# Kernel tuning notes

Measured on AMD Instinct MI355X. Metric: run time of the kernel, lower is better.

## Reference

```python
import jax, jax.numpy as jnp
import numpy as np


def setup_inputs() -> dict:
    key = jax.random.key(0)
    kx, kw = jax.random.split(key)
    x = jax.random.normal(kx, (32, 128, 64, 64), dtype=jnp.float32)
    weights = jax.random.normal(kw, (256, 128, 3, 3), dtype=jnp.float32) * 0.05
    return {"x": x, "weights": weights}


def reference(x, weights):
    # Valid-padding, stride-1, no-bias 2D cross-correlation, identical math
    # to the nested-loop HandmadeConv2d (sum over in_ch, kH, kW per output pixel).
    return jax.lax.conv_general_dilated(
        x, weights,
        window_strides=(1, 1),
        padding="VALID",
        dimension_numbers=("NCHW", "OIHW", "NCHW"),
    )
```

## Files before the change

kernel.cpp:

```cpp
#include <hip/hip_runtime.h>
#include <hip/hip_bf16.h>

typedef unsigned short ushort;
typedef unsigned int uint;
typedef __bf16 bf16x8 __attribute__((ext_vector_type(8)));
typedef float f32x4 __attribute__((ext_vector_type(4)));
typedef uint uint4v __attribute__((ext_vector_type(4)));
typedef uint uint2v __attribute__((ext_vector_type(2)));

#define CI 128
#define HIN 64
#define WIN 64
#define CO 256
#define HO 62
#define WO 62
#define NB 32
#define KTOT 1152
#define PIXIMG 3844
#define NPIX 123008
#define XIMG 524288
#define BK 64
#define NKT 18

__device__ __forceinline__ ushort f2bf(float f) {
  uint u = __builtin_bit_cast(uint, f);
  u += 0x7fffu + ((u >> 16) & 1u);
  return (ushort)(u >> 16);
}

__global__ void repack_w_kernel(const float* __restrict__ w, ushort* __restrict__ w2) {
  const int co = blockIdx.x;
  for (int idx = threadIdx.x; idx < KTOT; idx += 256) {
    const int t  = idx >> 7;
    const int ci = idx & 127;
    w2[co * KTOT + idx] = f2bf(w[(co * CI + ci) * 9 + t]);
  }
}

#define XPAD 132
__global__ __launch_bounds__(256) void repack_x_kernel(const float* __restrict__ x,
                                                       ushort* __restrict__ x2) {
  __shared__ float t[WIN * XPAD];
  const int n = blockIdx.y;
  const int h = blockIdx.x;
  const int tid = threadIdx.x;
  const float* src = x + ((size_t)n * CI * HIN + h) * WIN;
  #pragma unroll
  for (int it = 0; it < 8; ++it) {
    const int idx = it * 256 + tid;
    const int ci  = idx >> 4;
    const int w4  = (idx & 15) * 4;
    const float4 v = *reinterpret_cast<const float4*>(src + (size_t)ci * (HIN * WIN) + w4);
    t[(w4 + 0) * XPAD + ci] = v.x;
    t[(w4 + 1) * XPAD + ci] = v.y;
    t[(w4 + 2) * XPAD + ci] = v.z;
    t[(w4 + 3) * XPAD + ci] = v.w;
  }
  __syncthreads();
  ushort* dst = x2 + ((size_t)(n * HIN + h) * WIN) * CI;
  #pragma unroll
  for (int it = 0; it < 4; ++it) {
    const int idx = it * 256 + tid;
    const int w   = idx >> 4;
    const int cig = idx & 15;
    const float* p = &t[w * XPAD + cig * 8];
    uint4v q;
    q[0] = (uint)f2bf(p[0]) | ((uint)f2bf(p[1]) << 16);
    q[1] = (uint)f2bf(p[2]) | ((uint)f2bf(p[3]) << 16);
    q[2] = (uint)f2bf(p[4]) | ((uint)f2bf(p[5]) << 16);
    q[3] = (uint)f2bf(p[6]) | ((uint)f2bf(p[7]) << 16);
    *reinterpret_cast<uint4v*>(dst + (size_t)w * CI + cig * 8) = q;
  }
}

__global__ __launch_bounds__(256, 3)
void conv_nhwc_kernel(const ushort* __restrict__ x2, const ushort* __restrict__ w2,
                      float* __restrict__ out)
{
  __shared__ alignas(16) ushort a_lds[128 * 64];
  __shared__ alignas(16) ushort b_lds[128 * 64];

  const int tid  = threadIdx.x;
  const int lane = tid & 63;
  const int wid  = tid >> 6;
  const int wrow = wid >> 1;
  const int wcol = wid & 1;

  const int co0 = blockIdx.x * 128;
  const int p0  = blockIdx.y * 128;

  const int c4  = tid & 3;
  const int plA = tid >> 2;
  const int plB = plA + 64;
  int xbase[2];
  {
    int pls[2] = {plA, plB};
    #pragma unroll
    for (int i = 0; i < 2; ++i) {
      const int pglob = p0 + pls[i];
      const int nimg  = pglob / PIXIMG;
      const int prem  = pglob - nimg * PIXIMG;
      const int oh    = prem / WO;
      const int ow    = prem - oh * WO;
      xbase[i] = ((nimg * HIN + oh) * WIN + ow) * CI;
    }
  }
  const int dswA = plA * 64;
  const int dswB = plB * 64;

  const int arow_l = lane >> 3;
  const int achk_l = (lane & 7) ^ arow_l;
  const int asrc0  = (co0 + wid * 32 + arow_l) * KTOT + achk_l * 8;

  const int frow_a = wrow * 64 + (lane & 15);
  const int frow_b = wcol * 64 + (lane & 15);
  int aoff[2], boff[2];
  #pragma unroll
  for (int kk = 0; kk < 2; ++kk) {
    const int chk = (kk * 4 + (lane >> 4)) ^ (lane & 7);
    aoff[kk] = frow_a * 64 + chk * 8;
    boff[kk] = frow_b * 64 + chk * 8;
  }

  f32x4 acc[4][4];
  #pragma unroll
  for (int i = 0; i < 4; ++i)
    #pragma unroll
    for (int j = 0; j < 4; ++j)
      acc[i][j] = (f32x4){0.f, 0.f, 0.f, 0.f};

  for (int kt = 0; kt < NKT; ++kt) {
    const int k0 = kt * BK;
    if (kt) __syncthreads();

    #pragma unroll
    for (int i = 0; i < 4; ++i) {
      const ushort* src = w2 + asrc0 + i * (8 * KTOT) + k0;
      __builtin_amdgcn_global_load_lds(
          (const __attribute__((address_space(1))) uint*)(const void*)src,
          (__attribute__((address_space(3))) uint*)(void*)&a_lds[wid * 2048 + i * 512],
          16, 0, 0);
    }

    uint4v qb[4];
    int dsw[4];
    #pragma unroll
    for (int it = 0; it < 4; ++it) {
      const int kg  = c4 + (it & 1) * 4;
      const int gk  = kt * 8 + kg;
      const int t   = gk >> 4;
      const int cig = gk & 15;
      const int r   = (t * 11) >> 5;
      const int s   = t - r * 3;
      const int base = (it < 2) ? xbase[0] : xbase[1];
      qb[it] = *reinterpret_cast<const uint4v*>(x2 + (size_t)(base + (r * WIN + s) * CI + cig * 8));
      const int row = (it < 2) ? dswA : dswB;
      const int pl7 = ((it < 2) ? plA : plB) & 7;
      dsw[it] = row + ((kg ^ pl7) * 8);
    }
    #pragma unroll
    for (int it = 0; it < 4; ++it)
      *reinterpret_cast<uint4v*>(&b_lds[dsw[it]]) = qb[it];

    __syncthreads();

    #pragma unroll
    for (int kk = 0; kk < 2; ++kk) {
      bf16x8 af[4], bb[4];
      #pragma unroll
      for (int mi = 0; mi < 4; ++mi)
        af[mi] = *reinterpret_cast<const bf16x8*>(&a_lds[aoff[kk] + mi * (16 * 64)]);
      #pragma unroll
      for (int ni = 0; ni < 4; ++ni)
        bb[ni] = *reinterpret_cast<const bf16x8*>(&b_lds[boff[kk] + ni * (16 * 64)]);
      #pragma unroll
      for (int mi = 0; mi < 4; ++mi)
        #pragma unroll
        for (int ni = 0; ni < 4; ++ni)
          acc[mi][ni] = __builtin_amdgcn_mfma_f32_16x16x32_bf16(af[mi], bb[ni], acc[mi][ni], 0, 0, 0);
    }
  }

  #pragma unroll
  for (int ni = 0; ni < 4; ++ni) {
    const int pix = p0 + wcol * 64 + ni * 16 + (lane & 15);
    const int n2  = pix / PIXIMG;
    const int pr2 = pix - n2 * PIXIMG;
    float* ob = out + (size_t)n2 * (CO * PIXIMG) + pr2
                    + (size_t)(co0 + wrow * 64 + ((lane >> 4) * 4)) * PIXIMG;
    #pragma unroll
    for (int mi = 0; mi < 4; ++mi) {
      float* po = ob + (size_t)mi * (16 * PIXIMG);
      #pragma unroll
      for (int r = 0; r < 4; ++r)
        po[(size_t)r * PIXIMG] = acc[mi][ni][r];
    }
  }
}

__global__ __launch_bounds__(256, 3)
void conv_fallback_kernel(const float* __restrict__ x, const float* __restrict__ wt,
                          float* __restrict__ out)
{
  __shared__ alignas(16) ushort a_lds[128 * 64];
  __shared__ alignas(16) ushort b_lds[128 * 64];

  const int tid  = threadIdx.x;
  const int lane = tid & 63;
  const int wid  = tid >> 6;
  const int wrow = wid >> 1;
  const int wcol = wid & 1;
  const int co0 = blockIdx.x * 128;
  const int p0  = blockIdx.y * 128;

  const int pl    = tid & 127;
  const int kgsel = __builtin_amdgcn_readfirstlane(tid >> 7);
  const int pglob = p0 + pl;
  const int nimg  = pglob / PIXIMG;
  const int prem  = pglob - nimg * PIXIMG;
  const int oh    = prem / WO;
  const int ow    = prem - oh * WO;
  const int xpix  = nimg * XIMG + oh * WIN + ow;

  const int frow_a = wrow * 64 + (lane & 15);
  const int frow_b = wcol * 64 + (lane & 15);
  int aoff[2], boff[2];
  #pragma unroll
  for (int kk = 0; kk < 2; ++kk) {
    const int chk = (kk * 4 + (lane >> 4)) ^ (lane & 7);
    aoff[kk] = frow_a * 64 + chk * 8;
    boff[kk] = frow_b * 64 + chk * 8;
  }

  f32x4 acc[4][4];
  #pragma unroll
  for (int i = 0; i < 4; ++i)
    #pragma unroll
    for (int j = 0; j < 4; ++j)
      acc[i][j] = (f32x4){0.f, 0.f, 0.f, 0.f};

  for (int kt = 0; kt < NKT; ++kt) {
    const int k0 = kt * BK;
    if (kt) __syncthreads();

    #pragma unroll
    for (int it = 0; it < 4; ++it) {
      const int kg = kgsel + it * 2;
      uint pk[4];
      #pragma unroll
      for (int j = 0; j < 8; ++j) {
        const int k  = k0 + kg * 8 + j;
        const int ci = k / 9;
        const int rs = k - ci * 9;
        const int r  = rs / 3;
        const int s  = rs - r * 3;
        const ushort u = f2bf(x[xpix + ci * (HIN * WIN) + r * WIN + s]);
        if (j & 1) pk[j >> 1] |= ((uint)u) << 16;
        else       pk[j >> 1]  = (uint)u;
      }
      uint4v q = {pk[0], pk[1], pk[2], pk[3]};
      *reinterpret_cast<uint4v*>(&b_lds[pl * 64 + ((kg ^ (pl & 7)) * 8)]) = q;
    }

    #pragma unroll
    for (int i = 0; i < 8; ++i) {
      const int id  = i * 256 + tid;
      const int row = id >> 4;
      const int c4  = id & 15;
      const float4 v = *reinterpret_cast<const float4*>(
          wt + (size_t)(co0 + row) * KTOT + k0 + c4 * 4);
      uint2v q;
      q[0] = (uint)f2bf(v.x) | ((uint)f2bf(v.y) << 16);
      q[1] = (uint)f2bf(v.z) | ((uint)f2bf(v.w) << 16);
      *reinterpret_cast<uint2v*>(
          &a_lds[row * 64 + (((c4 >> 1) ^ (row & 7)) * 8) + (c4 & 1) * 4]) = q;
    }

    __syncthreads();

    #pragma unroll
    for (int kk = 0; kk < 2; ++kk) {
      bf16x8 af[4], bb[4];
      #pragma unroll
      for (int mi = 0; mi < 4; ++mi)
        af[mi] = *reinterpret_cast<const bf16x8*>(&a_lds[aoff[kk] + mi * (16 * 64)]);
      #pragma unroll
      for (int ni = 0; ni < 4; ++ni)
        bb[ni] = *reinterpret_cast<const bf16x8*>(&b_lds[boff[kk] + ni * (16 * 64)]);
      #pragma unroll
      for (int mi = 0; mi < 4; ++mi)
        #pragma unroll
        for (int ni = 0; ni < 4; ++ni)
          acc[mi][ni] = __builtin_amdgcn_mfma_f32_16x16x32_bf16(af[mi], bb[ni], acc[mi][ni], 0, 0, 0);
    }
  }

  #pragma unroll
  for (int ni = 0; ni < 4; ++ni) {
    const int pix = p0 + wcol * 64 + ni * 16 + (lane & 15);
    const int n2  = pix / PIXIMG;
    const int pr2 = pix - n2 * PIXIMG;
    float* ob = out + (size_t)n2 * (CO * PIXIMG) + pr2
                    + (size_t)(co0 + wrow * 64 + ((lane >> 4) * 4)) * PIXIMG;
    #pragma unroll
    for (int mi = 0; mi < 4; ++mi) {
      float* po = ob + (size_t)mi * (16 * PIXIMG);
      #pragma unroll
      for (int r = 0; r < 4; ++r)
        po[(size_t)r * PIXIMG] = acc[mi][ni][r];
    }
  }
}

extern "C" void kernel_launch(void* const* d_in, const int* in_sizes, int n_in,
                              void* d_out, int out_size, void* d_ws, size_t ws_size,
                              hipStream_t stream) {
  const float* x  = (const float*)d_in[0];
  const float* wt = (const float*)d_in[1];
  float* out = (float*)d_out;

  ushort* w2 = (ushort*)d_ws;
  ushort* x2 = (ushort*)((char*)d_ws + 589824);

  const size_t need = 589824 + (size_t)NB * XIMG * 2;

  if (ws_size >= need) {
    repack_w_kernel<<<dim3(CO), dim3(256), 0, stream>>>(wt, w2);
    repack_x_kernel<<<dim3(HIN, NB), dim3(256), 0, stream>>>(x, x2);
    conv_nhwc_kernel<<<dim3(CO / 128, NPIX / 128), dim3(256), 0, stream>>>(x2, w2, out);
  } else {
    conv_fallback_kernel<<<dim3(CO / 128, NPIX / 128), dim3(256), 0, stream>>>(x, wt, out);
  }
}
```

Baseline: 122.9 us.

## Load conv input tiles directly into LDS and remap blocks across XCDs

The B (input-patch) tile is now fetched with global_load_lds straight into shared memory instead of going through registers and ds_write, with per-lane row pointers precomputed once. The grid is flattened to 1D and remapped so that consecutive logical tiles (both output-channel halves of a pixel tile) land on the same XCD for L2 reuse. Launch bounds are raised to 4 blocks per CU and the K loop is fully unrolled. The goal is to cut register pressure and per-iteration address math and to raise occupancy, at the cost of more register constraints and a hardcoded block count.

```diff
diff --git a/kernel.cpp b/kernel.cpp
--- a/kernel.cpp
+++ b/kernel.cpp
@@ -73,7 +73,7 @@
   }
 }
 
-__global__ __launch_bounds__(256, 3)
+__global__ __launch_bounds__(256, 4)
 void conv_nhwc_kernel(const ushort* __restrict__ x2, const ushort* __restrict__ w2,
                       float* __restrict__ out)
 {
@@ -86,31 +86,28 @@
   const int wrow = wid >> 1;
   const int wcol = wid & 1;
 
-  const int co0 = blockIdx.x * 128;
-  const int p0  = blockIdx.y * 128;
-
-  const int c4  = tid & 3;
-  const int plA = tid >> 2;
-  const int plB = plA + 64;
-  int xbase[2];
-  {
-    int pls[2] = {plA, plB};
-    #pragma unroll
-    for (int i = 0; i < 2; ++i) {
-      const int pglob = p0 + pls[i];
-      const int nimg  = pglob / PIXIMG;
-      const int prem  = pglob - nimg * PIXIMG;
-      const int oh    = prem / WO;
-      const int ow    = prem - oh * WO;
-      xbase[i] = ((nimg * HIN + oh) * WIN + ow) * CI;
-    }
-  }
-  const int dswA = plA * 64;
-  const int dswB = plB * 64;
-
-  const int arow_l = lane >> 3;
-  const int achk_l = (lane & 7) ^ arow_l;
-  const int asrc0  = (co0 + wid * 32 + arow_l) * KTOT + achk_l * 8;
+  const int nwg = 1922, q8 = nwg >> 3, r8 = nwg & 7;
+  const int wg  = blockIdx.x;
+  const int xcd = wg & 7, sidx = wg >> 3;
+  const int logical = (xcd < r8 ? xcd * (q8 + 1) : r8 * (q8 + 1) + (xcd - r8) * q8) + sidx;
+  const int co0 = (logical & 1) * 128;
+  const int p0  = (logical >> 1) * 128;
+
+  const int lrow = lane >> 3;
+  const int lc   = (lane & 7) ^ lrow;
+
+  const ushort* pB[4];
+  #pragma unroll
+  for (int i = 0; i < 4; ++i) {
+    const int row   = wid * 32 + i * 8 + lrow;
+    const int pglob = p0 + row;
+    const int nimg  = pglob / PIXIMG;
+    const int prem  = pglob - nimg * PIXIMG;
+    const int oh    = prem / WO;
+    const int ow    = prem - oh * WO;
+    pB[i] = x2 + (size_t)((nimg * HIN + oh) * WIN + ow) * CI + lc * 8;
+  }
+  const ushort* pA = w2 + (size_t)(co0 + wid * 32 + lrow) * KTOT + lc * 8;
 
   const int frow_a = wrow * 64 + (lane & 15);
   const int frow_b = wcol * 64 + (lane & 15);
@@ -129,38 +126,32 @@
     for (int j = 0; j < 4; ++j)
       acc[i][j] = (f32x4){0.f, 0.f, 0.f, 0.f};
 
+  #pragma unroll
   for (int kt = 0; kt < NKT; ++kt) {
-    const int k0 = kt * BK;
     if (kt) __syncthreads();
 
+    const int tap   = kt >> 1;
+    const int rr    = (tap * 11) >> 5;
+    const int ss    = tap - rr * 3;
+    const int coffB = (rr * WIN + ss) * CI + (kt & 1) * 64;
+    const int coffA = kt * 64;
+
     #pragma unroll
     for (int i = 0; i < 4; ++i) {
-      const ushort* src = w2 + asrc0 + i * (8 * KTOT) + k0;
+      const ushort* src = pA + (size_t)i * (8 * KTOT) + coffA;
       __builtin_amdgcn_global_load_lds(
           (const __attribute__((address_space(1))) uint*)(const void*)src,
           (__attribute__((address_space(3))) uint*)(void*)&a_lds[wid * 2048 + i * 512],
           16, 0, 0);
     }
-
-    uint4v qb[4];
-    int dsw[4];
-    #pragma unroll
-    for (int it = 0; it < 4; ++it) {
-      const int kg  = c4 + (it & 1) * 4;
-      const int gk  = kt * 8 + kg;
-      const int t   = gk >> 4;
-      const int cig = gk & 15;
-      const int r   = (t * 11) >> 5;
-      const int s   = t - r * 3;
-      const int base = (it < 2) ? xbase[0] : xbase[1];
-      qb[it] = *reinterpret_cast<const uint4v*>(x2 + (size_t)(base + (r * WIN + s) * CI + cig * 8));
-      const int row = (it < 2) ? dswA : dswB;
-      const int pl7 = ((it < 2) ? plA : plB) & 7;
-      dsw[it] = row + ((kg ^ pl7) * 8);
-    }
-    #pragma unroll
-    for (int it = 0; it < 4; ++it)
-      *reinterpret_cast<uint4v*>(&b_lds[dsw[it]]) = qb[it];
+    #pragma unroll
+    for (int i = 0; i < 4; ++i) {
+      const ushort* src = pB[i] + coffB;
+      __builtin_amdgcn_global_load_lds(
+          (const __attribute__((address_space(1))) uint*)(const void*)src,
+          (__attribute__((address_space(3))) uint*)(void*)&b_lds[wid * 2048 + i * 512],
+          16, 0, 0);
+    }
 
     __syncthreads();
 
@@ -327,7 +318,7 @@
   if (ws_size >= need) {
     repack_w_kernel<<<dim3(CO), dim3(256), 0, stream>>>(wt, w2);
     repack_x_kernel<<<dim3(HIN, NB), dim3(256), 0, stream>>>(x, x2);
-    conv_nhwc_kernel<<<dim3(CO / 128, NPIX / 128), dim3(256), 0, stream>>>(x2, w2, out);
+    conv_nhwc_kernel<<<dim3(1922), dim3(256), 0, stream>>>(x2, w2, out);
   } else {
     conv_fallback_kernel<<<dim3(CO / 128, NPIX / 128), dim3(256), 0, stream>>>(x, wt, out);
   }
```

Result: faster. 104.7 us (-14.8%).
